# Performance work log

Hardware: AMD Instinct MI355X
Metric: run time of the kernel (lower is better)

Reference implementation:

```python
import jax, jax.numpy as jnp
import numpy as np

N = 8192
IN_F = 128
OUT_F = 64
ALPHA = 0.2  # LeakyReLU negative slope
NEG_INF = -1.0e9


def setup_inputs() -> dict:
    key = jax.random.key(0)
    k_x, k_adj, k_W, k_a = jax.random.split(key, 4)
    x = jax.random.normal(k_x, (N, IN_F), dtype=jnp.float32)
    adj = (jax.random.uniform(k_adj, (N, N)) < 0.02).astype(jnp.float32)
    adj = jnp.maximum(adj, jnp.eye(N, dtype=jnp.float32))
    W = jax.random.normal(k_W, (IN_F, OUT_F), dtype=jnp.float32) * (1.414 / np.sqrt(IN_F))
    a = jax.random.normal(k_a, (2 * OUT_F, 1), dtype=jnp.float32) * 0.1
    return {"x": x, "adj": adj, "W": W, "a": a}


def reference(x, adj, W, a):
    # h: [N, out_f]
    h = x @ W
    # GAT scores: e_ij = leakyrelu(a1.h_i + a2.h_j), dense [N, N]
    h_i = h @ a[:OUT_F]            # [N, 1]
    h_j = h @ a[OUT_F:]            # [N, 1]
    e = h_i + h_j.T                # [N, N]
    e = jax.nn.leaky_relu(e, negative_slope=ALPHA)
    # mask non-edges (adj <= 0) with -1e9, then row softmax
    attn_logits = jnp.where(adj > 0, e, NEG_INF)
    attn = jax.nn.softmax(attn_logits, axis=-1)
    # weighted aggregate + ELU (dropout is identity at p=0 / eval)
    out = jax.nn.elu(attn @ h)
    return out
```

## Files before the change

kernel.cpp:

```cpp
#include <hip/hip_runtime.h>
#include <hip/hip_bf16.h>

#define N_NODES 8192
#define IN_F 128
#define OUT_F 64
#define ALPHA 0.2f
#define CAP 512
#define WT_STRIDE 132

__global__ __launch_bounds__(256, 4) void gat_h(
    const float* __restrict__ x, const float* __restrict__ W,
    const float* __restrict__ a, float* __restrict__ h,
    float* __restrict__ hi, float* __restrict__ hj) {
  __shared__ float sWt[OUT_F][WT_STRIDE];
  int tid = threadIdx.x;
  for (int i = tid; i < IN_F * OUT_F; i += 256) {
    int k = i >> 6, f = i & 63;
    sWt[f][k] = W[i];
  }
  __syncthreads();

  int lane = tid & 63;
  int wid = tid >> 6;
  float a1 = a[lane], a2 = a[OUT_F + lane];
  int row0 = blockIdx.x * 8;

  for (int rr = 0; rr < 2; ++rr) {
    int row = row0 + rr * 4 + wid;
    const float4* xr = (const float4*)(x + (size_t)row * IN_F);
    float acc = 0.f;
#pragma unroll
    for (int k4 = 0; k4 < IN_F / 4; ++k4) {
      float4 xv = xr[k4];
      float4 wv = *(const float4*)&sWt[lane][k4 * 4];
      acc = fmaf(xv.x, wv.x, acc);
      acc = fmaf(xv.y, wv.y, acc);
      acc = fmaf(xv.z, wv.z, acc);
      acc = fmaf(xv.w, wv.w, acc);
    }
    h[(size_t)row * 64 + lane] = acc;
    float vi = acc * a1, vj = acc * a2;
#pragma unroll
    for (int o = 32; o >= 1; o >>= 1) {
      vi += __shfl_xor(vi, o);
      vj += __shfl_xor(vj, o);
    }
    if (lane == 0) { hi[row] = vi; hj[row] = vj; }
  }
}

__global__ __launch_bounds__(256, 4) void gat_row(
    const float* __restrict__ adj, const float* __restrict__ h,
    const float* __restrict__ hi, const float* __restrict__ hj,
    float* __restrict__ out) {
  __shared__ int s_idx[4][CAP];
  __shared__ float s_w[4][CAP];

  int tid = threadIdx.x;
  int lane = tid & 63;
  int wid = tid >> 6;
  int row = blockIdx.x * 4 + wid;

  const float4* arow = (const float4*)(adj + (size_t)row * N_NODES);
  unsigned int mask[4];
#pragma unroll
  for (int g = 0; g < 4; ++g) {
    unsigned int mk = 0;
#pragma unroll
    for (int it = 0; it < 8; ++it) {
      float4 vv = arow[lane + (g * 8 + it) * 64];
      mk |= (unsigned int)(vv.x > 0.f) << (it * 4 + 0);
      mk |= (unsigned int)(vv.y > 0.f) << (it * 4 + 1);
      mk |= (unsigned int)(vv.z > 0.f) << (it * 4 + 2);
      mk |= (unsigned int)(vv.w > 0.f) << (it * 4 + 3);
    }
    mask[g] = mk;
  }
  int c = __popc(mask[0]) + __popc(mask[1]) + __popc(mask[2]) + __popc(mask[3]);

  int incl = c;
#pragma unroll
  for (int o = 1; o < 64; o <<= 1) {
    int t = __shfl_up(incl, o);
    if (lane >= o) incl += t;
  }
  int off = incl - c;
  int cnt = __shfl(incl, 63);

  int* widx = s_idx[wid];
  float* ww = s_w[wid];
  float hii = hi[row];
  float lmax = -1e30f;
#pragma unroll
  for (int g = 0; g < 4; ++g) {
    unsigned int m = mask[g];
    while (m) {
      int b = __ffs(m) - 1;
      m &= m - 1;
      int j = ((lane + ((g * 8 + (b >> 2)) << 6)) << 2) + (b & 3);
      float l = hii + hj[j];
      l = (l > 0.f) ? l : ALPHA * l;
      if (off < CAP) { widx[off] = j; ww[off] = l; }
      ++off;
      lmax = fmaxf(lmax, l);
    }
  }

#pragma unroll
  for (int o = 32; o >= 1; o >>= 1) lmax = fmaxf(lmax, __shfl_xor(lmax, o));
  if (cnt > CAP) cnt = CAP;
  int cnt_pad = (cnt + 7) & ~7;

  float lsum = 0.f;
  for (int e = lane; e < cnt; e += 64) {
    float w = __expf(ww[e] - lmax);
    ww[e] = w;
    lsum += w;
  }
  if (cnt + lane < cnt_pad) { ww[cnt + lane] = 0.f; widx[cnt + lane] = 0; }
#pragma unroll
  for (int o = 32; o >= 1; o >>= 1) lsum += __shfl_xor(lsum, o);
  float inv = 1.f / lsum;

  float acc0 = 0.f, acc1 = 0.f, acc2 = 0.f, acc3 = 0.f;
  float acc4 = 0.f, acc5 = 0.f, acc6 = 0.f, acc7 = 0.f;
  for (int e = 0; e < cnt_pad; e += 8) {
    int4 ia = *(const int4*)&widx[e];
    int4 ib = *(const int4*)&widx[e + 4];
    float4 wa = *(const float4*)&ww[e];
    float4 wb = *(const float4*)&ww[e + 4];
    acc0 = fmaf(wa.x, h[(size_t)ia.x * 64 + lane], acc0);
    acc1 = fmaf(wa.y, h[(size_t)ia.y * 64 + lane], acc1);
    acc2 = fmaf(wa.z, h[(size_t)ia.z * 64 + lane], acc2);
    acc3 = fmaf(wa.w, h[(size_t)ia.w * 64 + lane], acc3);
    acc4 = fmaf(wb.x, h[(size_t)ib.x * 64 + lane], acc4);
    acc5 = fmaf(wb.y, h[(size_t)ib.y * 64 + lane], acc5);
    acc6 = fmaf(wb.z, h[(size_t)ib.z * 64 + lane], acc6);
    acc7 = fmaf(wb.w, h[(size_t)ib.w * 64 + lane], acc7);
  }
  float vv = ((acc0 + acc1) + (acc2 + acc3)) + ((acc4 + acc5) + (acc6 + acc7));
  vv *= inv;
  vv = (vv > 0.f) ? vv : expm1f(vv);
  out[(size_t)row * 64 + lane] = vv;
}

extern "C" void kernel_launch(void* const* d_in, const int* in_sizes, int n_in,
                              void* d_out, int out_size, void* d_ws, size_t ws_size,
                              hipStream_t stream) {
  const float* x   = (const float*)d_in[0];
  const float* adj = (const float*)d_in[1];
  const float* W   = (const float*)d_in[2];
  const float* a   = (const float*)d_in[3];
  float* out = (float*)d_out;

  float* h  = (float*)d_ws;
  float* hi = h + (size_t)N_NODES * OUT_F;
  float* hj = hi + N_NODES;

  gat_h<<<N_NODES / 8, 256, 0, stream>>>(x, W, a, h, hi, hj);
  gat_row<<<N_NODES / 4, 256, 0, stream>>>(adj, h, hi, hj, out);
}
```

Before: 101.0 us.

## Split adjacency scan into a wide compaction kernel and a separate aggregation kernel

Moves the dense adjacency scan into its own kernel. Each row is split across four 256-thread blocks, which compact edge indices into a per-row edge list using a wave prefix sum plus an atomic per-row counter. The aggregation kernel then reads the compact edge list, computes softmax weights without subtracting the row max, and gathers h. The aim is more memory-level parallelism on the 256MB adjacency read. The cost is an extra memset and kernel launch, an intermediate edge buffer, nondeterministic edge order, and some overflow risk in exp because the max is no longer subtracted.

```diff
diff --git a/kernel.cpp b/kernel.cpp
--- a/kernel.cpp
+++ b/kernel.cpp
@@ -49,10 +49,55 @@
   }
 }
 
-__global__ __launch_bounds__(256, 4) void gat_row(
-    const float* __restrict__ adj, const float* __restrict__ h,
-    const float* __restrict__ hi, const float* __restrict__ hj,
-    float* __restrict__ out) {
+__global__ __launch_bounds__(256) void gat_scan(
+    const float* __restrict__ adj, int* __restrict__ cnt,
+    int* __restrict__ edges) {
+  int tid = threadIdx.x;
+  int lane = tid & 63;
+  int row = blockIdx.x >> 2;
+  int seg = blockIdx.x & 3;
+  const float4* arow = (const float4*)(adj + (size_t)row * N_NODES) + seg * 512;
+
+  float4 v0 = arow[tid];
+  float4 v1 = arow[tid + 256];
+  unsigned int mk = 0;
+  mk |= (unsigned int)(v0.x > 0.f) << 0;
+  mk |= (unsigned int)(v0.y > 0.f) << 1;
+  mk |= (unsigned int)(v0.z > 0.f) << 2;
+  mk |= (unsigned int)(v0.w > 0.f) << 3;
+  mk |= (unsigned int)(v1.x > 0.f) << 4;
+  mk |= (unsigned int)(v1.y > 0.f) << 5;
+  mk |= (unsigned int)(v1.z > 0.f) << 6;
+  mk |= (unsigned int)(v1.w > 0.f) << 7;
+  int c = __popc(mk);
+
+  int incl = c;
+#pragma unroll
+  for (int o = 1; o < 64; o <<= 1) {
+    int t = __shfl_up(incl, o);
+    if (lane >= o) incl += t;
+  }
+  int base = 0;
+  if (lane == 63) base = atomicAdd(&cnt[row], incl);
+  base = __shfl(base, 63);
+  int off = base + incl - c;
+
+  int col0 = seg * 2048 + tid * 4;
+  int col1 = seg * 2048 + 1024 + tid * 4;
+  int* erow = edges + (size_t)row * CAP;
+  while (mk) {
+    int b = __ffs(mk) - 1;
+    mk &= mk - 1;
+    int j = (b < 4) ? (col0 + b) : (col1 + (b - 4));
+    if (off < CAP) erow[off] = j;
+    ++off;
+  }
+}
+
+__global__ __launch_bounds__(256, 4) void gat_agg(
+    const int* __restrict__ cnt, const int* __restrict__ edges,
+    const float* __restrict__ h, const float* __restrict__ hi,
+    const float* __restrict__ hj, float* __restrict__ out) {
   __shared__ int s_idx[4][CAP];
   __shared__ float s_w[4][CAP];
 
@@ -61,70 +106,32 @@
   int wid = tid >> 6;
   int row = blockIdx.x * 4 + wid;
 
-  const float4* arow = (const float4*)(adj + (size_t)row * N_NODES);
-  unsigned int mask[4];
-#pragma unroll
-  for (int g = 0; g < 4; ++g) {
-    unsigned int mk = 0;
-#pragma unroll
-    for (int it = 0; it < 8; ++it) {
-      float4 vv = arow[lane + (g * 8 + it) * 64];
-      mk |= (unsigned int)(vv.x > 0.f) << (it * 4 + 0);
-      mk |= (unsigned int)(vv.y > 0.f) << (it * 4 + 1);
-      mk |= (unsigned int)(vv.z > 0.f) << (it * 4 + 2);
-      mk |= (unsigned int)(vv.w > 0.f) << (it * 4 + 3);
-    }
-    mask[g] = mk;
-  }
-  int c = __popc(mask[0]) + __popc(mask[1]) + __popc(mask[2]) + __popc(mask[3]);
-
-  int incl = c;
-#pragma unroll
-  for (int o = 1; o < 64; o <<= 1) {
-    int t = __shfl_up(incl, o);
-    if (lane >= o) incl += t;
-  }
-  int off = incl - c;
-  int cnt = __shfl(incl, 63);
-
+  int cn = cnt[row];
+  if (cn > CAP) cn = CAP;
+  float hii = hi[row];
+  const int* erow = edges + (size_t)row * CAP;
   int* widx = s_idx[wid];
   float* ww = s_w[wid];
-  float hii = hi[row];
-  float lmax = -1e30f;
+
+  float psum = 0.f;
+  for (int e = lane; e < cn; e += 64) {
+    int j = erow[e];
+    float l = hii + hj[j];
+    l = (l > 0.f) ? l : ALPHA * l;
+    float w = __expf(l);
+    widx[e] = j;
+    ww[e] = w;
+    psum += w;
+  }
+  int cnp = (cn + 7) & ~7;
+  if (cn + lane < cnp) { ww[cn + lane] = 0.f; widx[cn + lane] = 0; }
 #pragma unroll
-  for (int g = 0; g < 4; ++g) {
-    unsigned int m = mask[g];
-    while (m) {
-      int b = __ffs(m) - 1;
-      m &= m - 1;
-      int j = ((lane + ((g * 8 + (b >> 2)) << 6)) << 2) + (b & 3);
-      float l = hii + hj[j];
-      l = (l > 0.f) ? l : ALPHA * l;
-      if (off < CAP) { widx[off] = j; ww[off] = l; }
-      ++off;
-      lmax = fmaxf(lmax, l);
-    }
-  }
-
-#pragma unroll
-  for (int o = 32; o >= 1; o >>= 1) lmax = fmaxf(lmax, __shfl_xor(lmax, o));
-  if (cnt > CAP) cnt = CAP;
-  int cnt_pad = (cnt + 7) & ~7;
-
-  float lsum = 0.f;
-  for (int e = lane; e < cnt; e += 64) {
-    float w = __expf(ww[e] - lmax);
-    ww[e] = w;
-    lsum += w;
-  }
-  if (cnt + lane < cnt_pad) { ww[cnt + lane] = 0.f; widx[cnt + lane] = 0; }
-#pragma unroll
-  for (int o = 32; o >= 1; o >>= 1) lsum += __shfl_xor(lsum, o);
-  float inv = 1.f / lsum;
+  for (int o = 32; o >= 1; o >>= 1) psum += __shfl_xor(psum, o);
+  float inv = 1.f / psum;
 
   float acc0 = 0.f, acc1 = 0.f, acc2 = 0.f, acc3 = 0.f;
   float acc4 = 0.f, acc5 = 0.f, acc6 = 0.f, acc7 = 0.f;
-  for (int e = 0; e < cnt_pad; e += 8) {
+  for (int e = 0; e < cnp; e += 8) {
     int4 ia = *(const int4*)&widx[e];
     int4 ib = *(const int4*)&widx[e + 4];
     float4 wa = *(const float4*)&ww[e];
@@ -153,10 +160,14 @@
   const float* a   = (const float*)d_in[3];
   float* out = (float*)d_out;
 
-  float* h  = (float*)d_ws;
-  float* hi = h + (size_t)N_NODES * OUT_F;
-  float* hj = hi + N_NODES;
+  float* h   = (float*)d_ws;
+  float* hi  = h + (size_t)N_NODES * OUT_F;
+  float* hj  = hi + N_NODES;
+  int*   cnt = (int*)(hj + N_NODES);
+  int*   edges = cnt + N_NODES;
 
+  hipMemsetAsync(cnt, 0, N_NODES * sizeof(int), stream);
   gat_h<<<N_NODES / 8, 256, 0, stream>>>(x, W, a, h, hi, hj);
-  gat_row<<<N_NODES / 4, 256, 0, stream>>>(adj, h, hi, hj, out);
+  gat_scan<<<N_NODES * 4, 256, 0, stream>>>(adj, cnt, edges);
+  gat_agg<<<N_NODES / 4, 256, 0, stream>>>(cnt, edges, h, hi, hj, out);
 }
```

After: 141.4 us. +40.0%, slower.

## Split each GAT row across a full block and drop softmax max pass

Applied to the files above, without the earlier changes.

Each row is now handled by a 256-thread block, with each of the four warps scanning a quarter of the adjacency columns and aggregating its own neighbor subset. Partial sums are combined through shared memory. The softmax max-subtraction pass is removed: exponentials are computed directly during the edge scan, and the per-warp edge buffer shrinks. This shortens per-warp serial loops and cuts shared memory, but adds block syncs and risks overflow if the logits become large.

```diff
diff --git a/kernel.cpp b/kernel.cpp
--- a/kernel.cpp
+++ b/kernel.cpp
@@ -5,7 +5,7 @@
 #define IN_F 128
 #define OUT_F 64
 #define ALPHA 0.2f
-#define CAP 512
+#define CAP 128
 #define WT_STRIDE 132
 
 __global__ __launch_bounds__(256, 4) void gat_h(
@@ -55,28 +55,25 @@
     float* __restrict__ out) {
   __shared__ int s_idx[4][CAP];
   __shared__ float s_w[4][CAP];
+  __shared__ float s_psum[4];
+  __shared__ float s_part[4][64];
 
   int tid = threadIdx.x;
   int lane = tid & 63;
   int wid = tid >> 6;
-  int row = blockIdx.x * 4 + wid;
+  int row = blockIdx.x;
 
-  const float4* arow = (const float4*)(adj + (size_t)row * N_NODES);
-  unsigned int mask[4];
+  const float4* aq = (const float4*)(adj + (size_t)row * N_NODES) + wid * 512;
+  unsigned int mk = 0;
 #pragma unroll
-  for (int g = 0; g < 4; ++g) {
-    unsigned int mk = 0;
-#pragma unroll
-    for (int it = 0; it < 8; ++it) {
-      float4 vv = arow[lane + (g * 8 + it) * 64];
-      mk |= (unsigned int)(vv.x > 0.f) << (it * 4 + 0);
-      mk |= (unsigned int)(vv.y > 0.f) << (it * 4 + 1);
-      mk |= (unsigned int)(vv.z > 0.f) << (it * 4 + 2);
-      mk |= (unsigned int)(vv.w > 0.f) << (it * 4 + 3);
-    }
-    mask[g] = mk;
+  for (int it = 0; it < 8; ++it) {
+    float4 vv = aq[lane + it * 64];
+    mk |= (unsigned int)(vv.x > 0.f) << (it * 4 + 0);
+    mk |= (unsigned int)(vv.y > 0.f) << (it * 4 + 1);
+    mk |= (unsigned int)(vv.z > 0.f) << (it * 4 + 2);
+    mk |= (unsigned int)(vv.w > 0.f) << (it * 4 + 3);
   }
-  int c = __popc(mask[0]) + __popc(mask[1]) + __popc(mask[2]) + __popc(mask[3]);
+  int c = __popc(mk);
 
   int incl = c;
 #pragma unroll
@@ -86,45 +83,34 @@
   }
   int off = incl - c;
   int cnt = __shfl(incl, 63);
+  if (cnt > CAP) cnt = CAP;
 
   int* widx = s_idx[wid];
   float* ww = s_w[wid];
   float hii = hi[row];
-  float lmax = -1e30f;
+  float psum = 0.f;
+  while (mk) {
+    int b = __ffs(mk) - 1;
+    mk &= mk - 1;
+    int j = (wid << 11) + (lane << 2) + ((b >> 2) << 8) + (b & 3);
+    float l = hii + hj[j];
+    l = (l > 0.f) ? l : ALPHA * l;
+    float w = __expf(l);
+    if (off < CAP) { widx[off] = j; ww[off] = w; }
+    ++off;
+    psum += w;
+  }
+  int cnp = (cnt + 7) & ~7;
+  if (lane < cnp - cnt) { ww[cnt + lane] = 0.f; widx[cnt + lane] = 0; }
 #pragma unroll
-  for (int g = 0; g < 4; ++g) {
-    unsigned int m = mask[g];
-    while (m) {
-      int b = __ffs(m) - 1;
-      m &= m - 1;
-      int j = ((lane + ((g * 8 + (b >> 2)) << 6)) << 2) + (b & 3);
-      float l = hii + hj[j];
-      l = (l > 0.f) ? l : ALPHA * l;
-      if (off < CAP) { widx[off] = j; ww[off] = l; }
-      ++off;
-      lmax = fmaxf(lmax, l);
-    }
-  }
-
-#pragma unroll
-  for (int o = 32; o >= 1; o >>= 1) lmax = fmaxf(lmax, __shfl_xor(lmax, o));
-  if (cnt > CAP) cnt = CAP;
-  int cnt_pad = (cnt + 7) & ~7;
-
-  float lsum = 0.f;
-  for (int e = lane; e < cnt; e += 64) {
-    float w = __expf(ww[e] - lmax);
-    ww[e] = w;
-    lsum += w;
-  }
-  if (cnt + lane < cnt_pad) { ww[cnt + lane] = 0.f; widx[cnt + lane] = 0; }
-#pragma unroll
-  for (int o = 32; o >= 1; o >>= 1) lsum += __shfl_xor(lsum, o);
-  float inv = 1.f / lsum;
+  for (int o = 32; o >= 1; o >>= 1) psum += __shfl_xor(psum, o);
+  if (lane == 0) s_psum[wid] = psum;
+  __syncthreads();
+  float inv = 1.f / (s_psum[0] + s_psum[1] + s_psum[2] + s_psum[3]);
 
   float acc0 = 0.f, acc1 = 0.f, acc2 = 0.f, acc3 = 0.f;
   float acc4 = 0.f, acc5 = 0.f, acc6 = 0.f, acc7 = 0.f;
-  for (int e = 0; e < cnt_pad; e += 8) {
+  for (int e = 0; e < cnp; e += 8) {
     int4 ia = *(const int4*)&widx[e];
     int4 ib = *(const int4*)&widx[e + 4];
     float4 wa = *(const float4*)&ww[e];
@@ -138,10 +124,15 @@
     acc6 = fmaf(wb.z, h[(size_t)ib.z * 64 + lane], acc6);
     acc7 = fmaf(wb.w, h[(size_t)ib.w * 64 + lane], acc7);
   }
-  float vv = ((acc0 + acc1) + (acc2 + acc3)) + ((acc4 + acc5) + (acc6 + acc7));
-  vv *= inv;
-  vv = (vv > 0.f) ? vv : expm1f(vv);
-  out[(size_t)row * 64 + lane] = vv;
+  s_part[wid][lane] =
+      ((acc0 + acc1) + (acc2 + acc3)) + ((acc4 + acc5) + (acc6 + acc7));
+  __syncthreads();
+  if (tid < 64) {
+    float vv = s_part[0][tid] + s_part[1][tid] + s_part[2][tid] + s_part[3][tid];
+    vv *= inv;
+    vv = (vv > 0.f) ? vv : expm1f(vv);
+    out[(size_t)row * 64 + tid] = vv;
+  }
 }
 
 extern "C" void kernel_launch(void* const* d_in, const int* in_sizes, int n_in,
@@ -158,5 +149,5 @@
   float* hj = hi + N_NODES;
 
   gat_h<<<N_NODES / 8, 256, 0, stream>>>(x, W, a, h, hi, hj);
-  gat_row<<<N_NODES / 4, 256, 0, stream>>>(adj, h, hi, hj, out);
+  gat_row<<<N_NODES, 256, 0, stream>>>(adj, h, hi, hj, out);
 }
```

After: 98.79 us. 1.02x faster.
